# Kernel tuning notes

Measured on AMD Instinct MI355X. Metric: run time of the kernel, lower is better.

The kernel has to match this reference:

```python
import math
import jax, jax.numpy as jnp
import numpy as np

IN_D = 16
H_DIM = 256
NB_STEPS = 50
B = 8192


def _cc_weights(nb_steps):
    # Clenshaw-Curtis quadrature weights and nodes, exactly as the torch code.
    k = np.arange(0, nb_steps + 1, dtype=np.float64).reshape(-1, 1)
    lam = np.cos(k @ k.T * math.pi / nb_steps)
    lam[:, 0] = 0.5
    lam[:, -1] = 0.5 * lam[:, -1]
    lam = lam * 2.0 / nb_steps
    W = np.arange(0, nb_steps + 1, dtype=np.float64).reshape(-1, 1)
    W[1::2] = 0.0
    W = 2.0 / (1.0 - W ** 2)
    W[0] = 1.0
    W[1::2] = 0.0
    cc = (lam.T @ W).astype(np.float32)  # [nb_steps+1, 1]
    steps = np.cos(np.arange(0, nb_steps + 1) * math.pi / nb_steps).astype(np.float32)  # [nb_steps+1]
    return jnp.asarray(cc), jnp.asarray(steps)


def setup_inputs() -> dict:
    key = jax.random.key(0)
    ks = jax.random.split(key, 16)
    s = 0.05
    return {
        "x": jax.random.normal(ks[0], (B, 1), jnp.float32),
        "h": jax.random.normal(ks[1], (B, IN_D - 1), jnp.float32),
        "iw1": jax.random.normal(ks[2], (H_DIM, IN_D), jnp.float32) * s,
        "ib1": jax.random.normal(ks[3], (H_DIM,), jnp.float32) * s,
        "iw2": jax.random.normal(ks[4], (H_DIM, H_DIM), jnp.float32) * s,
        "ib2": jax.random.normal(ks[5], (H_DIM,), jnp.float32) * s,
        "iw3": jax.random.normal(ks[6], (1, H_DIM), jnp.float32) * s,
        "ib3": jax.random.normal(ks[7], (1,), jnp.float32) * s,
        "nw1": jax.random.normal(ks[8], (H_DIM, IN_D - 1), jnp.float32) * s,
        "nb1": jax.random.normal(ks[9], (H_DIM,), jnp.float32) * s,
        "nw2": jax.random.normal(ks[10], (H_DIM, H_DIM), jnp.float32) * s,
        "nb2": jax.random.normal(ks[11], (H_DIM,), jnp.float32) * s,
        "nw3": jax.random.normal(ks[12], (2, H_DIM), jnp.float32) * s,
        "nb3": jax.random.normal(ks[13], (2,), jnp.float32) * s,
        "nb_steps": NB_STEPS,
    }


def _integrand(z, iw1, ib1, iw2, ib2, iw3, ib3):
    # IntegrandNN: Linear-ReLU-Linear-ReLU-Linear-ELU, then +1.0
    a = jax.nn.relu(z @ iw1.T + ib1)
    a = jax.nn.relu(a @ iw2.T + ib2)
    return jax.nn.elu(a @ iw3.T + ib3) + 1.0


def reference(x, h, iw1, ib1, iw2, ib2, iw3, ib3, nw1, nb1, nw2, nb2, nw3, nb3, nb_steps):
    cc, steps = _cc_weights(int(nb_steps))  # cc: [N+1,1], steps: [N+1]
    Bn, n_pts = x.shape[0], int(nb_steps) + 1
    # x0 = 0, so quadrature nodes X_k = x * (steps_k + 1) / 2 -> [B, N+1, 1]
    X = x[:, None, :] * ((steps[None, :, None] + 1.0) * 0.5)
    Xf = X.reshape(-1, 1)                                             # [B*(N+1), 1]
    Hf = jnp.broadcast_to(h[:, None, :], (Bn, n_pts, h.shape[1])).reshape(-1, h.shape[1])
    z = jnp.concatenate([Xf, Hf], axis=1)                             # [B*(N+1), in_d]
    f = _integrand(z, iw1, ib1, iw2, ib2, iw3, ib3).reshape(Bn, n_pts, 1)
    integral = jnp.sum(f * cc[None, :, :], axis=1) * x * 0.5          # [B, 1]
    # conditioner net on h: Linear-ReLU-Linear-ReLU-Linear -> [B, 2]
    a = jax.nn.relu(h @ nw1.T + nb1)
    a = jax.nn.relu(a @ nw2.T + nb2)
    out = a @ nw3.T + nb3
    offset = out[:, :1]
    scaling = jnp.exp(out[:, 1:2])
    return scaling * integral + offset
```

## Files before the change

kernel.cpp:

```cpp
#include <hip/hip_runtime.h>
#include <hip/hip_bf16.h>
#include <math.h>

#define BATCH 8192
#define HD    256
#define NPTS  51
#define MTOT  (BATCH*NPTS)

typedef __bf16 bf16x8 __attribute__((ext_vector_type(8)));
typedef float  f32x4  __attribute__((ext_vector_type(4)));

#define OFF_IW2P  0
#define OFF_W1X   131072
#define OFF_CC    132096
#define OFF_STEPS 132352
#define OFF_OFFS  132608
#define OFF_SCAL  165376
#define OFF_G1    198144
#define OFF_FV0   8586752
#define OFF_FV1   10257920

__device__ __forceinline__ unsigned short f2bf(float f) {
    union { float f; unsigned u; } v; v.f = f;
    unsigned r = v.u + 0x7FFFu + ((v.u >> 16) & 1u);
    return (unsigned short)(r >> 16);
}

__device__ __forceinline__ unsigned pk2bf(float lo, float hi) {
    __hip_bfloat162 t = __float22bfloat162_rn(float2{lo, hi});
    union { __hip_bfloat162 b; unsigned u; } v; v.b = t;
    return v.u;
}

__global__ void k1_fused(const float* __restrict__ iw2, const float* __restrict__ nw1,
                         const float* __restrict__ iw1, const float* __restrict__ ib1,
                         const float* __restrict__ nb1, const float* __restrict__ h,
                         const float* __restrict__ nw2, const float* __restrict__ nb2,
                         const float* __restrict__ nw3, const float* __restrict__ nb3,
                         unsigned short* iw2p, float* w1xs, float* cc, float* steps,
                         float* __restrict__ g1, float* __restrict__ offs,
                         float* __restrict__ scal) {
    int blk = blockIdx.x, tid = threadIdx.x;
    if (blk < 256) {
        int t = blk * 256 + tid;
        int n = t >> 8, k = t & 255;
        int half = n >> 7, nl = n & 127, c = k >> 3, j = k & 7;
        iw2p[half * 32768 + c * 1024 + nl * 8 + j] = f2bf(iw2[t]);
    } else if (blk == 256) {
        w1xs[tid] = iw1[tid * 16];
        const float PI_F = 3.14159265358979323846f;
        if (tid <= 50) {
            int j = tid;
            float s = 0.f;
            for (int i = 0; i <= 50; i += 2) {
                float w = (i == 0) ? 1.f : 2.f / (1.f - (float)(i * i));
                float l;
                if (j == 0 || j == 50) l = 0.5f;
                else { int r = (i * j) % 100; l = __cosf((float)r * (PI_F / 50.f)); }
                s += l * w;
            }
            cc[j]    = s * (2.f / 50.f);
            steps[j] = __cosf((float)j * (PI_F / 50.f));
        }
    } else {
        __shared__ float hs[16][15];
        __shared__ unsigned short a1s[16][264];
        __shared__ float Pp[4 * 2 * 16];
        int b0 = (blk - 257) * 16, n = tid;
        if (tid < 240) { int bb = tid / 15, j = tid % 15; hs[bb][j] = h[(b0 + bb) * 15 + j]; }
        __syncthreads();
        float ir[16], nr[15];
        const float4* ip = (const float4*)(iw1 + n * 16);
        ((float4*)ir)[0] = ip[0]; ((float4*)ir)[1] = ip[1];
        ((float4*)ir)[2] = ip[2]; ((float4*)ir)[3] = ip[3];
        #pragma unroll
        for (int j = 0; j < 15; ++j) nr[j] = nw1[n * 15 + j];
        float bi = ib1[n], bn = nb1[n];
        #pragma unroll
        for (int bb = 0; bb < 16; ++bb) {
            float g = bi, a = bn;
            #pragma unroll
            for (int j = 0; j < 15; ++j) { float hv = hs[bb][j]; g += hv * ir[j + 1]; a += hv * nr[j]; }
            g1[(b0 + bb) * 256 + n] = g;
            a1s[bb][n] = f2bf(fmaxf(a, 0.f));
        }
        __syncthreads();

        int lane = tid & 63, w = tid >> 6, l16 = lane & 15, quad = lane >> 4;
        f32x4 acc[4];
        #pragma unroll
        for (int nt = 0; nt < 4; ++nt) acc[nt] = (f32x4){0.f, 0.f, 0.f, 0.f};
        #pragma unroll
        for (int ks = 0; ks < 8; ++ks) {
            bf16x8 af = *(const bf16x8*)&a1s[l16][ks * 32 + quad * 8];
            #pragma unroll
            for (int nt = 0; nt < 4; ++nt) {
                const float* np = nw2 + (w * 64 + nt * 16 + l16) * 256 + ks * 32 + quad * 8;
                float4 f0 = ((const float4*)np)[0];
                float4 f1 = ((const float4*)np)[1];
                union { uint4 u; bf16x8 v; } bf;
                bf.u.x = pk2bf(f0.x, f0.y); bf.u.y = pk2bf(f0.z, f0.w);
                bf.u.z = pk2bf(f1.x, f1.y); bf.u.w = pk2bf(f1.z, f1.w);
                acc[nt] = __builtin_amdgcn_mfma_f32_16x16x32_bf16(af, bf.v, acc[nt], 0, 0, 0);
            }
        }
        float p0[4], p1[4];
        #pragma unroll
        for (int i = 0; i < 4; ++i) { p0[i] = 0.f; p1[i] = 0.f; }
        #pragma unroll
        for (int nt = 0; nt < 4; ++nt) {
            int nn = w * 64 + nt * 16 + l16;
            float bias = nb2[nn], wa = nw3[nn], wb = nw3[256 + nn];
            #pragma unroll
            for (int i = 0; i < 4; ++i) {
                float v = acc[nt][i] + bias;
                v = v > 0.f ? v : 0.f;
                p0[i] += v * wa;
                p1[i] += v * wb;
            }
        }
        #pragma unroll
        for (int mask = 1; mask < 16; mask <<= 1)
            #pragma unroll
            for (int i = 0; i < 4; ++i) {
                p0[i] += __shfl_xor(p0[i], mask, 64);
                p1[i] += __shfl_xor(p1[i], mask, 64);
            }
        if (l16 == 0) {
            #pragma unroll
            for (int i = 0; i < 4; ++i) {
                int r = quad * 4 + i;
                Pp[w * 32 + r]      = p0[i];
                Pp[w * 32 + 16 + r] = p1[i];
            }
        }
        __syncthreads();
        if (tid < 16) {
            float s0 = Pp[tid]      + Pp[32 + tid] + Pp[64 + tid] + Pp[96 + tid]  + nb3[0];
            float s1 = Pp[16 + tid] + Pp[48 + tid] + Pp[80 + tid] + Pp[112 + tid] + nb3[1];
            offs[b0 + tid] = s0;
            scal[b0 + tid] = __expf(s1);
        }
    }
}

__launch_bounds__(256, 4)
__global__ void k2_main(const float* __restrict__ x, const float* __restrict__ g1,
                        const float* __restrict__ w1xs, const unsigned short* __restrict__ iw2p,
                        const float* __restrict__ ib2, const float* __restrict__ iw3,
                        const float* __restrict__ steps,
                        float* __restrict__ fv0, float* __restrict__ fv1) {
    __shared__ __align__(16) unsigned char smem[37888];
    float* Pp = (float*)smem;

    int tid = threadIdx.x;
    int bid = blockIdx.x;
    int hf  = bid & 1;
    int m0  = (bid >> 1) * 128;
    int lane = tid & 63, w = tid >> 6;
    int l16 = lane & 15, quad = lane >> 4;

    unsigned blo = (unsigned)(((unsigned long long)(unsigned)m0 * 657931ull) >> 25);

    const unsigned char* bsrc = (const unsigned char*)iw2p + hf * 65536 + tid * 16;

    #pragma unroll
    for (int it = 0; it < 4; ++it)
        __builtin_amdgcn_global_load_lds(
            (const __attribute__((address_space(1))) unsigned int*)(bsrc + it * 4096),
            (__attribute__((address_space(3))) unsigned int*)(smem + tid * 16 + it * 4096),
            16, 0, 0);
    __builtin_amdgcn_global_load_lds(
        (const __attribute__((address_space(1))) unsigned int*)((const unsigned char*)(g1 + blo * 256) + tid * 16),
        (__attribute__((address_space(3))) unsigned int*)(smem + 32768 + tid * 16),
        16, 0, 0);
    if (w == 0)
        __builtin_amdgcn_global_load_lds(
            (const __attribute__((address_space(1))) unsigned int*)((const unsigned char*)w1xs + lane * 16),
            (__attribute__((address_space(3))) unsigned int*)(smem + 36864 + lane * 16),
            16, 0, 0);

    float xs_[2]; int rel_[2];
    #pragma unroll
    for (int mt = 0; mt < 2; ++mt) {
        int m = m0 + w * 32 + mt * 16 + l16;
        unsigned b = (unsigned)(((unsigned long long)(unsigned)m * 657931ull) >> 25);
        int p = m - (int)b * 51;
        xs_[mt] = x[b] * (steps[p] + 1.f) * 0.5f;
        rel_[mt] = (int)(b - blo) * 256;
    }

    f32x4 acc[2][8];
    #pragma unroll
    for (int mt = 0; mt < 2; ++mt)
        #pragma unroll
        for (int nt = 0; nt < 8; ++nt)
            acc[mt][nt] = (f32x4){0.f, 0.f, 0.f, 0.f};

    const float* Ag = (const float*)(smem + 32768);
    const float* Wl = (const float*)(smem + 36864);

    #pragma unroll
    for (int kc = 0; kc < 4; ++kc) {
        __syncthreads();
        if (kc < 3) {
            const unsigned char* s2 = bsrc + (kc + 1) * 16384;
            unsigned char* d2 = smem + ((kc + 1) & 1) * 16384 + tid * 16;
            #pragma unroll
            for (int it = 0; it < 4; ++it)
                __builtin_amdgcn_global_load_lds(
                    (const __attribute__((address_space(1))) unsigned int*)(s2 + it * 4096),
                    (__attribute__((address_space(3))) unsigned int*)(d2 + it * 4096),
                    16, 0, 0);
        }
        const unsigned short* Bl = (const unsigned short*)(smem + (kc & 1) * 16384);
        #pragma unroll
        for (int s = 0; s < 2; ++s) {
            int ks = kc * 2 + s;
            int ko = ks * 32 + quad * 8;
            int cl = s * 4 + quad;

            union { uint4 u; bf16x8 v; } af[2];
            {
                float4 w0 = ((const float4*)(Wl + ko))[0];
                float4 w1 = ((const float4*)(Wl + ko))[1];
                #pragma unroll
                for (int mt = 0; mt < 2; ++mt) {
                    const float* gp = Ag + rel_[mt] + ko;
                    float4 ga  = ((const float4*)gp)[0];
                    float4 gb2 = ((const float4*)gp)[1];
                    float xs = xs_[mt];
                    float a0 = fmaxf(ga.x  + xs * w0.x, 0.f);
                    float a1 = fmaxf(ga.y  + xs * w0.y, 0.f);
                    float a2 = fmaxf(ga.z  + xs * w0.z, 0.f);
                    float a3 = fmaxf(ga.w  + xs * w0.w, 0.f);
                    float a4 = fmaxf(gb2.x + xs * w1.x, 0.f);
                    float a5 = fmaxf(gb2.y + xs * w1.y, 0.f);
                    float a6 = fmaxf(gb2.z + xs * w1.z, 0.f);
                    float a7 = fmaxf(gb2.w + xs * w1.w, 0.f);
                    af[mt].u.x = pk2bf(a0, a1); af[mt].u.y = pk2bf(a2, a3);
                    af[mt].u.z = pk2bf(a4, a5); af[mt].u.w = pk2bf(a6, a7);
                }
            }

            #pragma unroll
            for (int g = 0; g < 2; ++g) {
                bf16x8 bfr[4];
                #pragma unroll
                for (int nt = 0; nt < 4; ++nt)
                    bfr[nt] = *(const bf16x8*)(Bl + (cl * 128 + (g * 4 + nt) * 16 + l16) * 8);
                #pragma unroll
                for (int mt = 0; mt < 2; ++mt)
                    #pragma unroll
                    for (int nt = 0; nt < 4; ++nt)
                        acc[mt][g * 4 + nt] = __builtin_amdgcn_mfma_f32_16x16x32_bf16(
                            af[mt].v, bfr[nt], acc[mt][g * 4 + nt], 0, 0, 0);
            }
        }
    }

    float pf[2][4];
    #pragma unroll
    for (int mt = 0; mt < 2; ++mt)
        #pragma unroll
        for (int i = 0; i < 4; ++i) pf[mt][i] = 0.f;
    #pragma unroll
    for (int nt = 0; nt < 8; ++nt) {
        int n = hf * 128 + nt * 16 + l16;
        float bias = ib2[n], w3 = iw3[n];
        #pragma unroll
        for (int mt = 0; mt < 2; ++mt)
            #pragma unroll
            for (int i = 0; i < 4; ++i) {
                float v = acc[mt][nt][i] + bias;
                v = v > 0.f ? v : 0.f;
                pf[mt][i] += v * w3;
            }
    }
    __syncthreads();
    #pragma unroll
    for (int mt = 0; mt < 2; ++mt)
        #pragma unroll
        for (int i = 0; i < 4; ++i) {
            int row = w * 32 + mt * 16 + quad * 4 + i;
            Pp[row * 20 + l16] = pf[mt][i];
        }
    __syncthreads();
    if (tid < 128) {
        const float4* pp = (const float4*)(Pp + tid * 20);
        float4 v0 = pp[0], v1 = pp[1], v2 = pp[2], v3 = pp[3];
        float s = v0.x + v0.y + v0.z + v0.w + v1.x + v1.y + v1.z + v1.w
                + v2.x + v2.y + v2.z + v2.w + v3.x + v3.y + v3.z + v3.w;
        (hf ? fv1 : fv0)[m0 + tid] = s;
    }
}

__global__ void k4_final(const float* __restrict__ x, const float* __restrict__ fv0,
                         const float* __restrict__ fv1, const float* __restrict__ ib3,
                         const float* __restrict__ cc,
                         const float* __restrict__ offs, const float* __restrict__ scal,
                         float* __restrict__ out) {
    int tid = threadIdx.x;
    int wv = tid >> 6, lane = tid & 63;
    int b = blockIdx.x * 4 + wv;
    float v = 0.f;
    if (lane < 51) {
        int m = b * 51 + lane;
        float s = fv0[m] + fv1[m] + ib3[0];
        float f = s > 0.f ? s + 1.f : __expf(s);
        v = f * cc[lane];
    }
    #pragma unroll
    for (int mask = 1; mask < 64; mask <<= 1) v += __shfl_xor(v, mask, 64);
    if (lane == 0)
        out[b] = scal[b] * (0.5f * x[b] * v) + offs[b];
}

extern "C" void kernel_launch(void* const* d_in, const int* in_sizes, int n_in,
                              void* d_out, int out_size, void* d_ws, size_t ws_size,
                              hipStream_t stream) {
    const float* x   = (const float*)d_in[0];
    const float* h   = (const float*)d_in[1];
    const float* iw1 = (const float*)d_in[2];
    const float* ib1 = (const float*)d_in[3];
    const float* iw2 = (const float*)d_in[4];
    const float* ib2 = (const float*)d_in[5];
    const float* iw3 = (const float*)d_in[6];
    const float* ib3 = (const float*)d_in[7];
    const float* nw1 = (const float*)d_in[8];
    const float* nb1 = (const float*)d_in[9];
    const float* nw2 = (const float*)d_in[10];
    const float* nb2 = (const float*)d_in[11];
    const float* nw3 = (const float*)d_in[12];
    const float* nb3 = (const float*)d_in[13];
    float* out = (float*)d_out;

    char* ws = (char*)d_ws;
    unsigned short* iw2p = (unsigned short*)(ws + OFF_IW2P);
    float* w1xs  = (float*)(ws + OFF_W1X);
    float* cc    = (float*)(ws + OFF_CC);
    float* steps = (float*)(ws + OFF_STEPS);
    float* offs  = (float*)(ws + OFF_OFFS);
    float* scal  = (float*)(ws + OFF_SCAL);
    float* g1    = (float*)(ws + OFF_G1);
    float* fv0   = (float*)(ws + OFF_FV0);
    float* fv1   = (float*)(ws + OFF_FV1);

    k1_fused<<<dim3(769), dim3(256), 0, stream>>>(iw2, nw1, iw1, ib1, nb1, h,
                                                  nw2, nb2, nw3, nb3,
                                                  iw2p, w1xs, cc, steps, g1, offs, scal);
    k2_main<<<dim3((MTOT / 128) * 2), dim3(256), 0, stream>>>(x, g1, w1xs, iw2p, ib2, iw3,
                                                              steps, fv0, fv1);
    k4_final<<<dim3(BATCH / 4), dim3(256), 0, stream>>>(x, fv0, fv1, ib3, cc, offs, scal, out);
}
```

Measured before the change: 165.3 us.

## Compute full 256-wide hidden layer per block instead of splitting N halves

Each k2 block now computes all 256 output columns for its 128 rows instead of splitting them into two blocks. The first-layer activations (ReLU of g1 + x*w1x, converted to bf16) are then built once per row tile rather than twice, and the separate fv0/fv1 partial buffers collapse into one. The cost is double the LDS per block (about 69 KB), twice the accumulator registers, and a lower occupancy target (launch bounds 2 instead of 4). Half as many blocks are launched.

```diff
diff --git a/kernel.cpp b/kernel.cpp
--- a/kernel.cpp
+++ b/kernel.cpp
@@ -17,8 +17,7 @@
 #define OFF_OFFS  132608
 #define OFF_SCAL  165376
 #define OFF_G1    198144
-#define OFF_FV0   8586752
-#define OFF_FV1   10257920
+#define OFF_FV    8586752
 
 __device__ __forceinline__ unsigned short f2bf(float f) {
     union { float f; unsigned u; } v; v.f = f;
@@ -144,40 +143,41 @@
     }
 }
 
-__launch_bounds__(256, 4)
+__launch_bounds__(256, 2)
 __global__ void k2_main(const float* __restrict__ x, const float* __restrict__ g1,
                         const float* __restrict__ w1xs, const unsigned short* __restrict__ iw2p,
                         const float* __restrict__ ib2, const float* __restrict__ iw3,
                         const float* __restrict__ steps,
-                        float* __restrict__ fv0, float* __restrict__ fv1) {
-    __shared__ __align__(16) unsigned char smem[37888];
+                        float* __restrict__ fv) {
+    __shared__ __align__(16) unsigned char smem[70656];
     float* Pp = (float*)smem;
 
     int tid = threadIdx.x;
     int bid = blockIdx.x;
-    int hf  = bid & 1;
-    int m0  = (bid >> 1) * 128;
+    int m0  = bid * 128;
     int lane = tid & 63, w = tid >> 6;
     int l16 = lane & 15, quad = lane >> 4;
 
     unsigned blo = (unsigned)(((unsigned long long)(unsigned)m0 * 657931ull) >> 25);
 
-    const unsigned char* bsrc = (const unsigned char*)iw2p + hf * 65536 + tid * 16;
-
-    #pragma unroll
-    for (int it = 0; it < 4; ++it)
-        __builtin_amdgcn_global_load_lds(
-            (const __attribute__((address_space(1))) unsigned int*)(bsrc + it * 4096),
-            (__attribute__((address_space(3))) unsigned int*)(smem + tid * 16 + it * 4096),
-            16, 0, 0);
+    const unsigned char* bbase = (const unsigned char*)iw2p;
+
+    #pragma unroll
+    for (int hf = 0; hf < 2; ++hf)
+        #pragma unroll
+        for (int it = 0; it < 4; ++it)
+            __builtin_amdgcn_global_load_lds(
+                (const __attribute__((address_space(1))) unsigned int*)(bbase + hf * 65536 + tid * 16 + it * 4096),
+                (__attribute__((address_space(3))) unsigned int*)(smem + hf * 16384 + tid * 16 + it * 4096),
+                16, 0, 0);
     __builtin_amdgcn_global_load_lds(
         (const __attribute__((address_space(1))) unsigned int*)((const unsigned char*)(g1 + blo * 256) + tid * 16),
-        (__attribute__((address_space(3))) unsigned int*)(smem + 32768 + tid * 16),
+        (__attribute__((address_space(3))) unsigned int*)(smem + 65536 + tid * 16),
         16, 0, 0);
     if (w == 0)
         __builtin_amdgcn_global_load_lds(
             (const __attribute__((address_space(1))) unsigned int*)((const unsigned char*)w1xs + lane * 16),
-            (__attribute__((address_space(3))) unsigned int*)(smem + 36864 + lane * 16),
+            (__attribute__((address_space(3))) unsigned int*)(smem + 69632 + lane * 16),
             16, 0, 0);
 
     float xs_[2]; int rel_[2];
@@ -190,30 +190,32 @@
         rel_[mt] = (int)(b - blo) * 256;
     }
 
-    f32x4 acc[2][8];
+    f32x4 acc[2][16];
     #pragma unroll
     for (int mt = 0; mt < 2; ++mt)
         #pragma unroll
-        for (int nt = 0; nt < 8; ++nt)
+        for (int nt = 0; nt < 16; ++nt)
             acc[mt][nt] = (f32x4){0.f, 0.f, 0.f, 0.f};
 
-    const float* Ag = (const float*)(smem + 32768);
-    const float* Wl = (const float*)(smem + 36864);
+    const float* Ag = (const float*)(smem + 65536);
+    const float* Wl = (const float*)(smem + 69632);
 
     #pragma unroll
     for (int kc = 0; kc < 4; ++kc) {
         __syncthreads();
         if (kc < 3) {
-            const unsigned char* s2 = bsrc + (kc + 1) * 16384;
-            unsigned char* d2 = smem + ((kc + 1) & 1) * 16384 + tid * 16;
-            #pragma unroll
-            for (int it = 0; it < 4; ++it)
-                __builtin_amdgcn_global_load_lds(
-                    (const __attribute__((address_space(1))) unsigned int*)(s2 + it * 4096),
-                    (__attribute__((address_space(3))) unsigned int*)(d2 + it * 4096),
-                    16, 0, 0);
-        }
-        const unsigned short* Bl = (const unsigned short*)(smem + (kc & 1) * 16384);
+            #pragma unroll
+            for (int hf = 0; hf < 2; ++hf) {
+                const unsigned char* s2 = bbase + hf * 65536 + (kc + 1) * 16384 + tid * 16;
+                unsigned char* d2 = smem + ((kc + 1) & 1) * 32768 + hf * 16384 + tid * 16;
+                #pragma unroll
+                for (int it = 0; it < 4; ++it)
+                    __builtin_amdgcn_global_load_lds(
+                        (const __attribute__((address_space(1))) unsigned int*)(s2 + it * 4096),
+                        (__attribute__((address_space(3))) unsigned int*)(d2 + it * 4096),
+                        16, 0, 0);
+            }
+        }
         #pragma unroll
         for (int s = 0; s < 2; ++s) {
             int ks = kc * 2 + s;
@@ -244,17 +246,21 @@
             }
 
             #pragma unroll
-            for (int g = 0; g < 2; ++g) {
-                bf16x8 bfr[4];
+            for (int hf = 0; hf < 2; ++hf) {
+                const unsigned short* Bl = (const unsigned short*)(smem + (kc & 1) * 32768 + hf * 16384);
                 #pragma unroll
-                for (int nt = 0; nt < 4; ++nt)
-                    bfr[nt] = *(const bf16x8*)(Bl + (cl * 128 + (g * 4 + nt) * 16 + l16) * 8);
-                #pragma unroll
-                for (int mt = 0; mt < 2; ++mt)
+                for (int g = 0; g < 2; ++g) {
+                    bf16x8 bfr[4];
                     #pragma unroll
                     for (int nt = 0; nt < 4; ++nt)
-                        acc[mt][g * 4 + nt] = __builtin_amdgcn_mfma_f32_16x16x32_bf16(
-                            af[mt].v, bfr[nt], acc[mt][g * 4 + nt], 0, 0, 0);
+                        bfr[nt] = *(const bf16x8*)(Bl + (cl * 128 + (g * 4 + nt) * 16 + l16) * 8);
+                    #pragma unroll
+                    for (int mt = 0; mt < 2; ++mt)
+                        #pragma unroll
+                        for (int nt = 0; nt < 4; ++nt)
+                            acc[mt][hf * 8 + g * 4 + nt] = __builtin_amdgcn_mfma_f32_16x16x32_bf16(
+                                af[mt].v, bfr[nt], acc[mt][hf * 8 + g * 4 + nt], 0, 0, 0);
+                }
             }
         }
     }
@@ -265,14 +271,14 @@
         #pragma unroll
         for (int i = 0; i < 4; ++i) pf[mt][i] = 0.f;
     #pragma unroll
-    for (int nt = 0; nt < 8; ++nt) {
-        int n = hf * 128 + nt * 16 + l16;
+    for (int idx = 0; idx < 16; ++idx) {
+        int n = idx * 16 + l16;
         float bias = ib2[n], w3 = iw3[n];
         #pragma unroll
         for (int mt = 0; mt < 2; ++mt)
             #pragma unroll
             for (int i = 0; i < 4; ++i) {
-                float v = acc[mt][nt][i] + bias;
+                float v = acc[mt][idx][i] + bias;
                 v = v > 0.f ? v : 0.f;
                 pf[mt][i] += v * w3;
             }
@@ -291,13 +297,12 @@
         float4 v0 = pp[0], v1 = pp[1], v2 = pp[2], v3 = pp[3];
         float s = v0.x + v0.y + v0.z + v0.w + v1.x + v1.y + v1.z + v1.w
                 + v2.x + v2.y + v2.z + v2.w + v3.x + v3.y + v3.z + v3.w;
-        (hf ? fv1 : fv0)[m0 + tid] = s;
-    }
-}
-
-__global__ void k4_final(const float* __restrict__ x, const float* __restrict__ fv0,
-                         const float* __restrict__ fv1, const float* __restrict__ ib3,
-                         const float* __restrict__ cc,
+        fv[m0 + tid] = s;
+    }
+}
+
+__global__ void k4_final(const float* __restrict__ x, const float* __restrict__ fv,
+                         const float* __restrict__ ib3, const float* __restrict__ cc,
                          const float* __restrict__ offs, const float* __restrict__ scal,
                          float* __restrict__ out) {
     int tid = threadIdx.x;
@@ -306,7 +311,7 @@
     float v = 0.f;
     if (lane < 51) {
         int m = b * 51 + lane;
-        float s = fv0[m] + fv1[m] + ib3[0];
+        float s = fv[m] + ib3[0];
         float f = s > 0.f ? s + 1.f : __expf(s);
         v = f * cc[lane];
     }
@@ -343,13 +348,12 @@
     float* offs  = (float*)(ws + OFF_OFFS);
     float* scal  = (float*)(ws + OFF_SCAL);
     float* g1    = (float*)(ws + OFF_G1);
-    float* fv0   = (float*)(ws + OFF_FV0);
-    float* fv1   = (float*)(ws + OFF_FV1);
+    float* fv    = (float*)(ws + OFF_FV);
 
     k1_fused<<<dim3(769), dim3(256), 0, stream>>>(iw2, nw1, iw1, ib1, nb1, h,
                                                   nw2, nb2, nw3, nb3,
                                                   iw2p, w1xs, cc, steps, g1, offs, scal);
-    k2_main<<<dim3((MTOT / 128) * 2), dim3(256), 0, stream>>>(x, g1, w1xs, iw2p, ib2, iw3,
-                                                              steps, fv0, fv1);
-    k4_final<<<dim3(BATCH / 4), dim3(256), 0, stream>>>(x, fv0, fv1, ib3, cc, offs, scal, out);
-}
+    k2_main<<<dim3(MTOT / 128), dim3(256), 0, stream>>>(x, g1, w1xs, iw2p, ib2, iw3,
+                                                        steps, fv);
+    k4_final<<<dim3(BATCH / 4), dim3(256), 0, stream>>>(x, fv, ib3, cc, offs, scal, out);
+}
```

Result: faster. 158.0 us (-4.4%).

## Move conditioner net into main kernel and recompute first-layer h projection in-block

Applied to the files above, without the earlier changes.

The conditioner MLP blocks move from the prep kernel into extra leading blocks of the main kernel. The per-batch first-layer h projection (g1) is no longer written to global memory and reloaded. Each main block now recomputes it for its up-to-4 batch rows directly into shared memory. This drops an 8 MB global intermediate and shortens the prep kernel on the critical path, at the cost of redundant FMA work and scalar h loads in every main block.

```diff
diff --git a/kernel.cpp b/kernel.cpp
--- a/kernel.cpp
+++ b/kernel.cpp
@@ -16,7 +16,6 @@
 #define OFF_STEPS 132352
 #define OFF_OFFS  132608
 #define OFF_SCAL  165376
-#define OFF_G1    198144
 #define OFF_FV0   8586752
 #define OFF_FV1   10257920
 
@@ -32,21 +31,15 @@
     return v.u;
 }
 
-__global__ void k1_fused(const float* __restrict__ iw2, const float* __restrict__ nw1,
-                         const float* __restrict__ iw1, const float* __restrict__ ib1,
-                         const float* __restrict__ nb1, const float* __restrict__ h,
-                         const float* __restrict__ nw2, const float* __restrict__ nb2,
-                         const float* __restrict__ nw3, const float* __restrict__ nb3,
-                         unsigned short* iw2p, float* w1xs, float* cc, float* steps,
-                         float* __restrict__ g1, float* __restrict__ offs,
-                         float* __restrict__ scal) {
+__global__ void k1_prep(const float* __restrict__ iw2, const float* __restrict__ iw1,
+                        unsigned short* iw2p, float* w1xs, float* cc, float* steps) {
     int blk = blockIdx.x, tid = threadIdx.x;
     if (blk < 256) {
         int t = blk * 256 + tid;
         int n = t >> 8, k = t & 255;
         int half = n >> 7, nl = n & 127, c = k >> 3, j = k & 7;
         iw2p[half * 32768 + c * 1024 + nl * 8 + j] = f2bf(iw2[t]);
-    } else if (blk == 256) {
+    } else {
         w1xs[tid] = iw1[tid * 16];
         const float PI_F = 3.14159265358979323846f;
         if (tid <= 50) {
@@ -62,76 +55,95 @@
             cc[j]    = s * (2.f / 50.f);
             steps[j] = __cosf((float)j * (PI_F / 50.f));
         }
-    } else {
-        __shared__ float hs[16][15];
-        __shared__ unsigned short a1s[16][264];
-        __shared__ float Pp[4 * 2 * 16];
-        int b0 = (blk - 257) * 16, n = tid;
-        if (tid < 240) { int bb = tid / 15, j = tid % 15; hs[bb][j] = h[(b0 + bb) * 15 + j]; }
+    }
+}
+
+__launch_bounds__(256, 4)
+__global__ void k2_main(const float* __restrict__ x,
+                        const float* __restrict__ w1xs, const unsigned short* __restrict__ iw2p,
+                        const float* __restrict__ ib2, const float* __restrict__ iw3,
+                        const float* __restrict__ steps,
+                        const float* __restrict__ h, const float* __restrict__ iw1,
+                        const float* __restrict__ ib1,
+                        const float* __restrict__ nw1, const float* __restrict__ nb1,
+                        const float* __restrict__ nw2, const float* __restrict__ nb2,
+                        const float* __restrict__ nw3, const float* __restrict__ nb3,
+                        float* __restrict__ offs, float* __restrict__ scal,
+                        float* __restrict__ fv0, float* __restrict__ fv1) {
+    __shared__ __align__(16) unsigned char smem[37888];
+    int tid = threadIdx.x, bid = blockIdx.x;
+    int lane = tid & 63, w = tid >> 6;
+    int l16 = lane & 15, quad = lane >> 4;
+
+    if (bid < 512) {
+        float* hs = (float*)smem;
+        unsigned short* a1s = (unsigned short*)(smem + 1024);
+        float* Pp = (float*)(smem + 10240);
+        int b0 = bid * 16;
+        if (tid < 240) { int bb = tid / 15, j = tid % 15; hs[bb * 15 + j] = h[(b0 + bb) * 15 + j]; }
         __syncthreads();
-        float ir[16], nr[15];
-        const float4* ip = (const float4*)(iw1 + n * 16);
-        ((float4*)ir)[0] = ip[0]; ((float4*)ir)[1] = ip[1];
-        ((float4*)ir)[2] = ip[2]; ((float4*)ir)[3] = ip[3];
-        #pragma unroll
-        for (int j = 0; j < 15; ++j) nr[j] = nw1[n * 15 + j];
-        float bi = ib1[n], bn = nb1[n];
-        #pragma unroll
-        for (int bb = 0; bb < 16; ++bb) {
-            float g = bi, a = bn;
-            #pragma unroll
-            for (int j = 0; j < 15; ++j) { float hv = hs[bb][j]; g += hv * ir[j + 1]; a += hv * nr[j]; }
-            g1[(b0 + bb) * 256 + n] = g;
-            a1s[bb][n] = f2bf(fmaxf(a, 0.f));
+        {
+            int n = tid;
+            float nr[15];
+            #pragma unroll
+            for (int j = 0; j < 15; ++j) nr[j] = nw1[n * 15 + j];
+            float bn = nb1[n];
+            #pragma unroll
+            for (int bb = 0; bb < 16; ++bb) {
+                float a = bn;
+                #pragma unroll
+                for (int j = 0; j < 15; ++j) a += hs[bb * 15 + j] * nr[j];
+                a1s[bb * 264 + n] = f2bf(fmaxf(a, 0.f));
+            }
         }
         __syncthreads();
-
-        int lane = tid & 63, w = tid >> 6, l16 = lane & 15, quad = lane >> 4;
-        f32x4 acc[4];
-        #pragma unroll
-        for (int nt = 0; nt < 4; ++nt) acc[nt] = (f32x4){0.f, 0.f, 0.f, 0.f};
-        #pragma unroll
-        for (int ks = 0; ks < 8; ++ks) {
-            bf16x8 af = *(const bf16x8*)&a1s[l16][ks * 32 + quad * 8];
+        {
+            f32x4 acc[4];
+            #pragma unroll
+            for (int nt = 0; nt < 4; ++nt) acc[nt] = (f32x4){0.f, 0.f, 0.f, 0.f};
+            #pragma unroll
+            for (int ks = 0; ks < 8; ++ks) {
+                bf16x8 af = *(const bf16x8*)&a1s[l16 * 264 + ks * 32 + quad * 8];
+                #pragma unroll
+                for (int nt = 0; nt < 4; ++nt) {
+                    const float* np = nw2 + (w * 64 + nt * 16 + l16) * 256 + ks * 32 + quad * 8;
+                    float4 f0 = ((const float4*)np)[0];
+                    float4 f1 = ((const float4*)np)[1];
+                    union { uint4 u; bf16x8 v; } bf;
+                    bf.u.x = pk2bf(f0.x, f0.y); bf.u.y = pk2bf(f0.z, f0.w);
+                    bf.u.z = pk2bf(f1.x, f1.y); bf.u.w = pk2bf(f1.z, f1.w);
+                    acc[nt] = __builtin_amdgcn_mfma_f32_16x16x32_bf16(af, bf.v, acc[nt], 0, 0, 0);
+                }
+            }
+            float p0[4], p1[4];
+            #pragma unroll
+            for (int i = 0; i < 4; ++i) { p0[i] = 0.f; p1[i] = 0.f; }
             #pragma unroll
             for (int nt = 0; nt < 4; ++nt) {
-                const float* np = nw2 + (w * 64 + nt * 16 + l16) * 256 + ks * 32 + quad * 8;
-                float4 f0 = ((const float4*)np)[0];
-                float4 f1 = ((const float4*)np)[1];
-                union { uint4 u; bf16x8 v; } bf;
-                bf.u.x = pk2bf(f0.x, f0.y); bf.u.y = pk2bf(f0.z, f0.w);
-                bf.u.z = pk2bf(f1.x, f1.y); bf.u.w = pk2bf(f1.z, f1.w);
-                acc[nt] = __builtin_amdgcn_mfma_f32_16x16x32_bf16(af, bf.v, acc[nt], 0, 0, 0);
-            }
-        }
-        float p0[4], p1[4];
-        #pragma unroll
-        for (int i = 0; i < 4; ++i) { p0[i] = 0.f; p1[i] = 0.f; }
-        #pragma unroll
-        for (int nt = 0; nt < 4; ++nt) {
-            int nn = w * 64 + nt * 16 + l16;
-            float bias = nb2[nn], wa = nw3[nn], wb = nw3[256 + nn];
-            #pragma unroll
-            for (int i = 0; i < 4; ++i) {
-                float v = acc[nt][i] + bias;
-                v = v > 0.f ? v : 0.f;
-                p0[i] += v * wa;
-                p1[i] += v * wb;
-            }
-        }
-        #pragma unroll
-        for (int mask = 1; mask < 16; mask <<= 1)
-            #pragma unroll
-            for (int i = 0; i < 4; ++i) {
-                p0[i] += __shfl_xor(p0[i], mask, 64);
-                p1[i] += __shfl_xor(p1[i], mask, 64);
-            }
-        if (l16 == 0) {
-            #pragma unroll
-            for (int i = 0; i < 4; ++i) {
-                int r = quad * 4 + i;
-                Pp[w * 32 + r]      = p0[i];
-                Pp[w * 32 + 16 + r] = p1[i];
+                int nn = w * 64 + nt * 16 + l16;
+                float bias = nb2[nn], wa = nw3[nn], wb = nw3[256 + nn];
+                #pragma unroll
+                for (int i = 0; i < 4; ++i) {
+                    float v = acc[nt][i] + bias;
+                    v = v > 0.f ? v : 0.f;
+                    p0[i] += v * wa;
+                    p1[i] += v * wb;
+                }
+            }
+            #pragma unroll
+            for (int mask = 1; mask < 16; mask <<= 1)
+                #pragma unroll
+                for (int i = 0; i < 4; ++i) {
+                    p0[i] += __shfl_xor(p0[i], mask, 64);
+                    p1[i] += __shfl_xor(p1[i], mask, 64);
+                }
+            if (l16 == 0) {
+                #pragma unroll
+                for (int i = 0; i < 4; ++i) {
+                    int r = quad * 4 + i;
+                    Pp[w * 32 + r]      = p0[i];
+                    Pp[w * 32 + 16 + r] = p1[i];
+                }
             }
         }
         __syncthreads();
@@ -141,24 +153,13 @@
             offs[b0 + tid] = s0;
             scal[b0 + tid] = __expf(s1);
         }
-    }
-}
-
-__launch_bounds__(256, 4)
-__global__ void k2_main(const float* __restrict__ x, const float* __restrict__ g1,
-                        const float* __restrict__ w1xs, const unsigned short* __restrict__ iw2p,
-                        const float* __restrict__ ib2, const float* __restrict__ iw3,
-                        const float* __restrict__ steps,
-                        float* __restrict__ fv0, float* __restrict__ fv1) {
-    __shared__ __align__(16) unsigned char smem[37888];
+        return;
+    }
+
+    int gb = bid - 512;
+    int hf = gb & 1;
+    int m0 = (gb >> 1) * 128;
     float* Pp = (float*)smem;
-
-    int tid = threadIdx.x;
-    int bid = blockIdx.x;
-    int hf  = bid & 1;
-    int m0  = (bid >> 1) * 128;
-    int lane = tid & 63, w = tid >> 6;
-    int l16 = lane & 15, quad = lane >> 4;
 
     unsigned blo = (unsigned)(((unsigned long long)(unsigned)m0 * 657931ull) >> 25);
 
@@ -170,15 +171,28 @@
             (const __attribute__((address_space(1))) unsigned int*)(bsrc + it * 4096),
             (__attribute__((address_space(3))) unsigned int*)(smem + tid * 16 + it * 4096),
             16, 0, 0);
-    __builtin_amdgcn_global_load_lds(
-        (const __attribute__((address_space(1))) unsigned int*)((const unsigned char*)(g1 + blo * 256) + tid * 16),
-        (__attribute__((address_space(3))) unsigned int*)(smem + 32768 + tid * 16),
-        16, 0, 0);
     if (w == 0)
         __builtin_amdgcn_global_load_lds(
             (const __attribute__((address_space(1))) unsigned int*)((const unsigned char*)w1xs + lane * 16),
             (__attribute__((address_space(3))) unsigned int*)(smem + 36864 + lane * 16),
             16, 0, 0);
+
+    {
+        float ir[16];
+        const float4* ip = (const float4*)(iw1 + tid * 16);
+        ((float4*)ir)[0] = ip[0]; ((float4*)ir)[1] = ip[1];
+        ((float4*)ir)[2] = ip[2]; ((float4*)ir)[3] = ip[3];
+        float bi = ib1[tid];
+        float* Agw = (float*)(smem + 32768);
+        #pragma unroll
+        for (int bb = 0; bb < 4; ++bb) {
+            int bidx = (int)blo + bb; if (bidx > BATCH - 1) bidx = BATCH - 1;
+            float g = bi;
+            #pragma unroll
+            for (int j = 0; j < 15; ++j) g += h[bidx * 15 + j] * ir[j + 1];
+            Agw[bb * 256 + tid] = g;
+        }
+    }
 
     float xs_[2]; int rel_[2];
     #pragma unroll
@@ -342,14 +356,12 @@
     float* steps = (float*)(ws + OFF_STEPS);
     float* offs  = (float*)(ws + OFF_OFFS);
     float* scal  = (float*)(ws + OFF_SCAL);
-    float* g1    = (float*)(ws + OFF_G1);
     float* fv0   = (float*)(ws + OFF_FV0);
     float* fv1   = (float*)(ws + OFF_FV1);
 
-    k1_fused<<<dim3(769), dim3(256), 0, stream>>>(iw2, nw1, iw1, ib1, nb1, h,
-                                                  nw2, nb2, nw3, nb3,
-                                                  iw2p, w1xs, cc, steps, g1, offs, scal);
-    k2_main<<<dim3((MTOT / 128) * 2), dim3(256), 0, stream>>>(x, g1, w1xs, iw2p, ib2, iw3,
-                                                              steps, fv0, fv1);
+    k1_prep<<<dim3(257), dim3(256), 0, stream>>>(iw2, iw1, iw2p, w1xs, cc, steps);
+    k2_main<<<dim3(512 + (MTOT / 128) * 2), dim3(256), 0, stream>>>(
+        x, w1xs, iw2p, ib2, iw3, steps, h, iw1, ib1,
+        nw1, nb1, nw2, nb2, nw3, nb3, offs, scal, fv0, fv1);
     k4_final<<<dim3(BATCH / 4), dim3(256), 0, stream>>>(x, fv0, fv1, ib3, cc, offs, scal, out);
 }
```

Measured after the change: 158.9 us. -3.9%, faster.
